# Kernel tuning notes

Measured on AMD Instinct MI355X. Metric: run time of the kernel, lower is better.

The kernel has to match this reference:

```python
import jax, jax.numpy as jnp
import numpy as np

C = 128; H = 56; W = 56; WS = 7; SS = 3; NH = 4; T = 8; B = 4
BT = B * T; L = H * W; N = WS * WS; HD = C // NH; SCALE = HD ** -0.5
NW = (H // WS) * (W // WS)

def _np_consts():
    # spatial relative position index (Swin)
    coords = np.stack(np.meshgrid(np.arange(WS), np.arange(WS), indexing='ij')).reshape(2, -1)
    rel = (coords[:, :, None] - coords[:, None, :]).transpose(1, 2, 0)
    rel[..., 0] += WS - 1; rel[..., 1] += WS - 1; rel[..., 0] *= 2 * WS - 1
    rpi = rel.sum(-1)  # (N, N) in [0, (2WS-1)^2)
    # temporal relative index
    tri = (np.arange(T)[:, None] - np.arange(T)[None, :]) + T - 1  # (T, T)
    # shifted-window attention mask
    img = np.zeros((1, H, W, 1), np.float32); cnt = 0
    sl = (slice(0, -WS), slice(-WS, -SS), slice(-SS, None))
    for hs in sl:
        for ws_ in sl:
            img[:, hs, ws_, :] = cnt; cnt += 1
    mw = img.reshape(1, H // WS, WS, W // WS, WS, 1).transpose(0, 1, 3, 2, 4, 5).reshape(-1, N)
    am = mw[:, None, :] - mw[:, :, None]
    attn_mask = np.where(am != 0, -100.0, 0.0).astype(np.float32)  # (NW, N, N)
    return rpi, tri, attn_mask

RPI, TRI, ATTN_MASK_NP = _np_consts()

def _ln(x, g, b, eps=1e-5):
    m = x.mean(-1, keepdims=True)
    v = ((x - m) ** 2).mean(-1, keepdims=True)
    return (x - m) * jax.lax.rsqrt(v + eps) * g + b

def _attn(x, bias, mask, qkv_w, qkv_b, proj_w, proj_b):
    # x: (Bn, n, C); bias: (NH, n, n); mask: (NW, n, n) or None
    Bn, n, _ = x.shape
    qkv = (x @ qkv_w + qkv_b).reshape(Bn, n, 3, NH, HD).transpose(2, 0, 3, 1, 4)
    q, k, v = qkv[0] * SCALE, qkv[1], qkv[2]  # (Bn, NH, n, HD)
    a = jnp.einsum('bhnd,bhmd->bhnm', q, k) + bias[None]
    if mask is not None:
        nW = mask.shape[0]
        a = (a.reshape(Bn // nW, nW, NH, n, n) + mask[None, :, None]).reshape(Bn, NH, n, n)
    a = jax.nn.softmax(a, axis=-1)
    o = jnp.einsum('bhnm,bhmd->bhnd', a, v).transpose(0, 2, 1, 3).reshape(Bn, n, C)
    return o @ proj_w + proj_b

def _fwd(x, qkv_w, qkv_b, proj_w, proj_b, rpb_table, tpb_table,
         norm1_g, norm1_b, norm2_g, norm2_b,
         mlp_w1, mlp_b1, mlp_w2, mlp_b2,
         s_w1, s_b1, s_w2, s_b2,
         t_w1, t_b1, t_w2, t_b2,
         a_w1, a_b1, a_w2, a_b2):
    gelu = lambda z: jax.nn.gelu(z, approximate=False)
    mask = jnp.asarray(ATTN_MASK_NP)
    sp_bias = rpb_table[RPI.reshape(-1)].reshape(N, N, NH).transpose(2, 0, 1)  # (NH,N,N)
    tp_bias = tpb_table[TRI.reshape(-1)].reshape(T, T, NH).transpose(2, 0, 1)  # (NH,T,T)

    # ---- temporal attention (t_attn=True, signal='video') ----
    shortcut = x
    xt = x.reshape(B, T, L, C).transpose(0, 2, 1, 3).reshape(B * L, T, C)
    xt = _ln(xt, norm1_g, norm1_b)
    xt = _attn(xt, tp_bias, None, qkv_w, qkv_b, proj_w, proj_b)
    # T_Adapter (non-residual)
    xt = gelu(xt @ t_w1 + t_b1) @ t_w2 + t_b2
    xt = xt.reshape(B, L, T, C).transpose(0, 2, 1, 3).reshape(BT, L, C)
    x = shortcut + xt

    # ---- shifted-window spatial attention ----
    shortcut = x
    xs = _ln(x, norm1_g, norm1_b).reshape(BT, H, W, C)
    xs = jnp.roll(xs, (-SS, -SS), axis=(1, 2))
    # window partition -> (BT*NW, N, C)
    xw = xs.reshape(BT, H // WS, WS, W // WS, WS, C).transpose(0, 1, 3, 2, 4, 5).reshape(-1, N, C)
    aw = _attn(xw, sp_bias, mask, qkv_w, qkv_b, proj_w, proj_b)
    # S_Adapter (SAdapter2, residual inside)
    aw = aw + (gelu(aw @ s_w1 + s_b1) @ s_w2 + s_b2)
    # window reverse
    xs = aw.reshape(BT, H // WS, W // WS, WS, WS, C).transpose(0, 1, 3, 2, 4, 5).reshape(BT, H, W, C)
    xs = jnp.roll(xs, (SS, SS), axis=(1, 2)).reshape(BT, L, C)
    x = shortcut + xs

    # ---- MLP + MLP_Adapter (AIM-style, scaled 0.5) ----
    xn = _ln(x, norm2_g, norm2_b)
    mlp = (gelu(xn @ mlp_w1 + mlp_b1)) @ mlp_w2 + mlp_b2
    ada = (gelu(xn @ a_w1 + a_b1)) @ a_w2 + a_b2
    return x + mlp + 0.5 * ada

def setup_inputs() -> dict:
    key = jax.random.key(0)
    ks = iter(jax.random.split(key, 16))
    p = lambda *s: jax.random.normal(next(ks), s, jnp.float32) * 0.02
    Ah = C // 4; M = 4 * C
    return {
        'x': jax.random.normal(next(ks), (BT, L, C), jnp.float32),
        'qkv_w': p(C, 3 * C), 'qkv_b': jnp.zeros((3 * C,), jnp.float32),
        'proj_w': p(C, C), 'proj_b': jnp.zeros((C,), jnp.float32),
        'rpb_table': p((2 * WS - 1) ** 2, NH), 'tpb_table': p(2 * T - 1, NH),
        'norm1_g': jnp.ones((C,), jnp.float32), 'norm1_b': jnp.zeros((C,), jnp.float32),
        'norm2_g': jnp.ones((C,), jnp.float32), 'norm2_b': jnp.zeros((C,), jnp.float32),
        'mlp_w1': p(C, M), 'mlp_b1': jnp.zeros((M,), jnp.float32),
        'mlp_w2': p(M, C), 'mlp_b2': jnp.zeros((C,), jnp.float32),
        's_w1': p(C, Ah), 's_b1': jnp.zeros((Ah,), jnp.float32),
        's_w2': p(Ah, C), 's_b2': jnp.zeros((C,), jnp.float32),
        't_w1': p(C, Ah), 't_b1': jnp.zeros((Ah,), jnp.float32),
        't_w2': p(Ah, C), 't_b2': jnp.zeros((C,), jnp.float32),
        'a_w1': p(C, Ah), 'a_b1': jnp.zeros((Ah,), jnp.float32),
        'a_w2': p(Ah, C), 'a_b2': jnp.zeros((C,), jnp.float32),
    }

def reference(x, qkv_w, qkv_b, proj_w, proj_b, rpb_table, tpb_table,
              norm1_g, norm1_b, norm2_g, norm2_b,
              mlp_w1, mlp_b1, mlp_w2, mlp_b2,
              s_w1, s_b1, s_w2, s_b2,
              t_w1, t_b1, t_w2, t_b2,
              a_w1, a_b1, a_w2, a_b2):
    return _fwd(x, qkv_w, qkv_b, proj_w, proj_b, rpb_table, tpb_table,
                norm1_g, norm1_b, norm2_g, norm2_b,
                mlp_w1, mlp_b1, mlp_w2, mlp_b2,
                s_w1, s_b1, s_w2, s_b2,
                t_w1, t_b1, t_w2, t_b2,
                a_w1, a_b1, a_w2, a_b2)
```

## Files before the change

### kernel.cpp

```cpp
#include <hip/hip_runtime.h>

#define TOKS 100352
#define LDIM 3136
#define SCALE_F 0.17677669529663687f

typedef unsigned short u16;
typedef u16   u16x8 __attribute__((ext_vector_type(8)));
typedef short s16x8 __attribute__((ext_vector_type(8)));
typedef float f32x8 __attribute__((ext_vector_type(8)));
typedef float f32x4 __attribute__((ext_vector_type(4)));

__device__ __forceinline__ float bf2f(u16 u){ return __uint_as_float(((unsigned)u)<<16); }
__device__ __forceinline__ u16 f2bf(float f){
  unsigned u = __float_as_uint(f);
  return (u16)((u + 0x7FFFu + ((u>>16)&1u)) >> 16);
}
__device__ __forceinline__ unsigned cvtpk(float a, float b){
  unsigned r;
  asm("v_cvt_pk_bf16_f32 %0, %1, %2" : "=v"(r) : "v"(a), "v"(b));
  return r;
}
__device__ __forceinline__ f32x8 ldbf8(const u16* p){
  u16x8 u = *(const u16x8*)p;
  f32x8 f;
  #pragma unroll
  for (int j=0;j<8;j++) f[j] = bf2f(u[j]);
  return f;
}
__device__ __forceinline__ u16x8 pack8(f32x8 v){
  u16x8 r;
  #pragma unroll
  for (int j=0;j<8;j++) r[j] = f2bf(v[j]);
  return r;
}
__device__ __forceinline__ float sum8(f32x8 a){
  return ((a[0]+a[1])+(a[2]+a[3]))+((a[4]+a[5])+(a[6]+a[7]));
}
__device__ __forceinline__ float gelu_f(float x){
  return x / (1.0f + __expf(-1.702f*x));
}

__device__ __forceinline__ void gl16(const u16* g, u16* l){
  __builtin_amdgcn_global_load_lds(
      (const __attribute__((address_space(1))) unsigned*)(const void*)g,
      (__attribute__((address_space(3))) unsigned*)(void*)l, 16, 0, 0);
}
__device__ __forceinline__ void stage_tile(const u16* __restrict__ src, size_t rowstart,
    int KTOT, int koff, u16* lds, int wv, int lane){
  const int rr = wv*4 + (lane>>4);
  const int sl = lane&15;
  const int kb = sl ^ (rr&7);
  const u16* g0 = src + (rowstart + rr)*(size_t)KTOT + koff + kb*8;
  u16* l0 = lds + wv*4*128;
  #pragma unroll
  for (int it=0; it<8; it++)
    gl16(g0 + (size_t)it*16*KTOT, l0 + it*16*128);
}

struct WSrc { const float* p[10]; };
__global__ __launch_bounds__(256) void prep_w(WSrc s, u16* __restrict__ dst){
  const int Ks[10]={128,128,128,512,128,32,128,32,128,32};
  const int Ns[10]={384,128,512,128,32,128,32,128,32,128};
  const int off[11]={0,49152,65536,131072,196608,200704,204800,208896,212992,217088,221184};
  int idx = blockIdx.x*256+threadIdx.x;
  int m=0;
  #pragma unroll
  for (int i=0;i<10;i++) if (idx>=off[i+1]) m=i+1;
  int e = idx-off[m];
  int K=Ks[m], Nn=Ns[m];
  int n=e/K, k=e-n*K;
  dst[idx] = f2bf(s.p[m][k*Nn+n]);
}

__global__ __launch_bounds__(256) void ln_kernel(const float* __restrict__ x,
    const float* __restrict__ g, const float* __restrict__ bta, u16* __restrict__ out)
{
  int tok  = (int)((blockIdx.x*256u + threadIdx.x) >> 6);
  int lane = threadIdx.x & 63;
  const float* xr = x + (size_t)tok*128;
  float v0 = xr[lane], v1 = xr[lane+64];
  float s = v0+v1;
  #pragma unroll
  for (int o=32;o;o>>=1) s += __shfl_xor(s,o);
  float m = s*(1.0f/128.0f);
  float d0=v0-m, d1=v1-m;
  float q = d0*d0+d1*d1;
  #pragma unroll
  for (int o=32;o;o>>=1) q += __shfl_xor(q,o);
  float rs = rsqrtf(q*(1.0f/128.0f)+1e-5f);
  u16* orow = out + (size_t)tok*128;
  orow[lane]    = f2bf(d0*rs*g[lane]   + bta[lane]);
  orow[lane+64] = f2bf(d1*rs*g[lane+64]+ bta[lane+64]);
}

template<int KCH, int NTC, int EPI>
__global__ __launch_bounds__(256,2) void gemm_tile(
    const u16* __restrict__ X, const u16* __restrict__ WT,
    const float* __restrict__ bias, void* outp, int N,
    const float* res1, const u16* __restrict__ adab)
{
  constexpr int KTOT = KCH*128;
  __shared__ u16 As[128*128];
  __shared__ u16 Bs[128*128];
  const int tid = threadIdx.x;
  const int wv = tid>>6, lane = tid&63, lr = lane>>4, lc = lane&15;
  const int wr = wv>>1, wc = wv&1;
  const size_t row0 = (size_t)blockIdx.x*128;

  f32x4 acc[4][4];
  #pragma unroll
  for (int mi=0;mi<4;mi++)
    #pragma unroll
    for (int nj=0;nj<4;nj++) acc[mi][nj] = (f32x4){0.f,0.f,0.f,0.f};

  for (int kc=0; kc<KCH; kc++){
    for (int nt=0; nt<NTC; nt++){
      if (kc+nt > 0) __syncthreads();
      if (nt == 0) stage_tile(X, row0, KTOT, kc*128, As, wv, lane);
      stage_tile(WT, (size_t)nt*128, KTOT, kc*128, Bs, wv, lane);
      __syncthreads();
      #pragma unroll
      for (int kt=0; kt<4; kt++){
        s16x8 af[4], bfr[4];
        #pragma unroll
        for (int mi=0;mi<4;mi++){
          int row = wr*64 + mi*16 + lc;
          af[mi] = *(const s16x8*)&As[row*128 + (((kt*4+lr) ^ (lc&7))*8)];
        }
        #pragma unroll
        for (int nj=0;nj<4;nj++){
          int col = wc*64 + nj*16 + lc;
          bfr[nj] = *(const s16x8*)&Bs[col*128 + (((kt*4+lr) ^ (lc&7))*8)];
        }
        #pragma unroll
        for (int mi=0;mi<4;mi++)
          #pragma unroll
          for (int nj=0;nj<4;nj++)
            acc[mi][nj] = __builtin_amdgcn_mfma_f32_16x16x32_bf16(bfr[nj], af[mi], acc[mi][nj], 0,0,0);
      }
      {
        #pragma unroll
        for (int nj=0;nj<4;nj++){
          const int colb = nt*128 + wc*64 + nj*16 + lr*4;
          float4 b4 = *(const float4*)&bias[colb];
          #pragma unroll
          for (int mi=0;mi<4;mi++){
            const size_t row = row0 + wr*64 + mi*16 + lc;
            float v0=acc[mi][nj][0]+b4.x, v1=acc[mi][nj][1]+b4.y,
                  v2=acc[mi][nj][2]+b4.z, v3=acc[mi][nj][3]+b4.w;
            if constexpr (EPI==1){ v0=gelu_f(v0); v1=gelu_f(v1); v2=gelu_f(v2); v3=gelu_f(v3); }
            uint2 pk; pk.x = cvtpk(v0,v1); pk.y = cvtpk(v2,v3);
            *(uint2*)&((u16*)outp)[row*(size_t)N + colb] = pk;
            acc[mi][nj] = (f32x4){0.f,0.f,0.f,0.f};
          }
        }
      }
    }
  }
  (void)res1; (void)adab;
}

template<int SMODE>
__global__ __launch_bounds__(256,2) void proj_ada_tile(
    const u16* __restrict__ O, const u16* __restrict__ PW, const float* __restrict__ pb,
    const u16* __restrict__ W1T, const float* __restrict__ b1,
    const u16* __restrict__ W2T, const float* __restrict__ b2,
    const float* __restrict__ res1, float* __restrict__ outp,
    const float* __restrict__ gn, const float* __restrict__ gb, u16* __restrict__ xnout)
{
  __shared__ u16 As[128*128];
  __shared__ u16 Bs[128*128];
  __shared__ u16 Hs[4][32][40];
  const int tid = threadIdx.x;
  const int wv = tid>>6, lane = tid&63, lr = lane>>4, lc = lane&15;
  const int wr = wv>>1, wc = wv&1;
  const size_t row0 = (size_t)blockIdx.x*128;
  stage_tile(O, row0, 128, 0, As, wv, lane);
  stage_tile(PW, 0, 128, 0, Bs, wv, lane);
  __syncthreads();
  f32x4 acc[4][4];
  #pragma unroll
  for (int mi=0;mi<4;mi++)
    #pragma unroll
    for (int nj=0;nj<4;nj++) acc[mi][nj] = (f32x4){0.f,0.f,0.f,0.f};
  #pragma unroll
  for (int kt=0; kt<4; kt++){
    s16x8 af[4], bfr[4];
    #pragma unroll
    for (int mi=0;mi<4;mi++)
      af[mi] = *(const s16x8*)&As[(wr*64+mi*16+lc)*128 + (((kt*4+lr) ^ (lc&7))*8)];
    #pragma unroll
    for (int nj=0;nj<4;nj++)
      bfr[nj] = *(const s16x8*)&Bs[(wc*64+nj*16+lc)*128 + (((kt*4+lr) ^ (lc&7))*8)];
    #pragma unroll
    for (int mi=0;mi<4;mi++)
      #pragma unroll
      for (int nj=0;nj<4;nj++)
        acc[mi][nj] = __builtin_amdgcn_mfma_f32_16x16x32_bf16(bfr[nj], af[mi], acc[mi][nj], 0,0,0);
  }
  __syncthreads();
  #pragma unroll
  for (int nj=0;nj<4;nj++){
    const int colb = wc*64 + nj*16 + lr*4;
    float4 b4 = *(const float4*)&pb[colb];
    #pragma unroll
    for (int mi=0;mi<4;mi++){
      const int row = wr*64 + mi*16 + lc;
      uint2 pk;
      pk.x = cvtpk(acc[mi][nj][0]+b4.x, acc[mi][nj][1]+b4.y);
      pk.y = cvtpk(acc[mi][nj][2]+b4.z, acc[mi][nj][3]+b4.w);
      *(uint2*)&As[row*128 + (((colb>>3) ^ (row&7))*8) + (colb&7)] = pk;
    }
  }
  __syncthreads();
  const int rbase = wv*32;
  f32x4 a2[2][2];
  #pragma unroll
  for (int mi=0;mi<2;mi++){ a2[mi][0]=(f32x4){0.f,0.f,0.f,0.f}; a2[mi][1]=(f32x4){0.f,0.f,0.f,0.f}; }
  #pragma unroll
  for (int kt=0; kt<4; kt++){
    s16x8 af0 = *(const s16x8*)&As[(rbase+lc)*128 + (((kt*4+lr) ^ (lc&7))*8)];
    s16x8 af1 = *(const s16x8*)&As[(rbase+16+lc)*128 + (((kt*4+lr) ^ (lc&7))*8)];
    #pragma unroll
    for (int nj=0; nj<2; nj++){
      s16x8 b = *(const s16x8*)&W1T[(size_t)(nj*16+lc)*128 + kt*32 + lr*8];
      a2[0][nj] = __builtin_amdgcn_mfma_f32_16x16x32_bf16(b, af0, a2[0][nj], 0,0,0);
      a2[1][nj] = __builtin_amdgcn_mfma_f32_16x16x32_bf16(b, af1, a2[1][nj], 0,0,0);
    }
  }
  #pragma unroll
  for (int nj=0;nj<2;nj++){
    const int hb = nj*16 + lr*4;
    float4 b4 = *(const float4*)&b1[hb];
    #pragma unroll
    for (int mi=0;mi<2;mi++){
      const int tok = mi*16 + lc;
      uint2 pk;
      pk.x = cvtpk(gelu_f(a2[mi][nj][0]+b4.x), gelu_f(a2[mi][nj][1]+b4.y));
      pk.y = cvtpk(gelu_f(a2[mi][nj][2]+b4.z), gelu_f(a2[mi][nj][3]+b4.w));
      *(uint2*)&Hs[wv][tok][hb] = pk;
    }
  }
  f32x4 a3[2][8];
  #pragma unroll
  for (int mi=0;mi<2;mi++){
    s16x8 af = *(const s16x8*)&Hs[wv][mi*16+lc][lr*8];
    #pragma unroll
    for (int nj=0;nj<8;nj++){
      s16x8 b = *(const s16x8*)&W2T[(size_t)(nj*16+lc)*32 + lr*8];
      a3[mi][nj] = __builtin_amdgcn_mfma_f32_16x16x32_bf16(b, af, (f32x4){0.f,0.f,0.f,0.f}, 0,0,0);
    }
  }
  float sum[2]={0.f,0.f}, sq[2]={0.f,0.f};
  #pragma unroll
  for (int mi=0;mi<2;mi++){
    const int rl = rbase + mi*16 + lc;
    const size_t row = row0 + rl;
    #pragma unroll
    for (int nj=0;nj<8;nj++){
      const int colb = nj*16 + lr*4;
      float4 b4 = *(const float4*)&b2[colb];
      float4 r4 = *(const float4*)&res1[row*128 + colb];
      f32x4 v;
      v[0]=a3[mi][nj][0]+b4.x+r4.x; v[1]=a3[mi][nj][1]+b4.y+r4.y;
      v[2]=a3[mi][nj][2]+b4.z+r4.z; v[3]=a3[mi][nj][3]+b4.w+r4.w;
      if constexpr (SMODE==1){
        uint2 pu = *(const uint2*)&As[rl*128 + (((colb>>3) ^ (rl&7))*8) + (colb&7)];
        v[0] += bf2f((u16)(pu.x&0xffff)); v[1] += bf2f((u16)(pu.x>>16));
        v[2] += bf2f((u16)(pu.y&0xffff)); v[3] += bf2f((u16)(pu.y>>16));
      }
      float4 st; st.x=v[0]; st.y=v[1]; st.z=v[2]; st.w=v[3];
      *(float4*)&outp[row*128 + colb] = st;
      a3[mi][nj] = v;
      sum[mi] += (v[0]+v[1])+(v[2]+v[3]);
      sq[mi]  += (v[0]*v[0]+v[1]*v[1])+(v[2]*v[2]+v[3]*v[3]);
    }
  }
  #pragma unroll
  for (int mi=0;mi<2;mi++){
    float s2 = sum[mi], q2 = sq[mi];
    s2 += __shfl_xor(s2,16); s2 += __shfl_xor(s2,32);
    q2 += __shfl_xor(q2,16); q2 += __shfl_xor(q2,32);
    float mean = s2*(1.0f/128.0f);
    float var  = q2*(1.0f/128.0f) - mean*mean;
    float rs   = rsqrtf(var + 1e-5f);
    const size_t row = row0 + rbase + mi*16 + lc;
    #pragma unroll
    for (int nj=0;nj<8;nj++){
      const int colb = nj*16 + lr*4;
      float4 g4 = *(const float4*)&gn[colb];
      float4 h4 = *(const float4*)&gb[colb];
      uint2 pk;
      pk.x = cvtpk((a3[mi][nj][0]-mean)*rs*g4.x + h4.x,
                   (a3[mi][nj][1]-mean)*rs*g4.y + h4.y);
      pk.y = cvtpk((a3[mi][nj][2]-mean)*rs*g4.z + h4.z,
                   (a3[mi][nj][3]-mean)*rs*g4.w + h4.w);
      *(uint2*)&xnout[row*128 + colb] = pk;
    }
  }
}

__global__ __launch_bounds__(256,2) void mlp_fused(
    const u16* __restrict__ X, const u16* __restrict__ W1T, const float* __restrict__ b1,
    const u16* __restrict__ W2T, const float* __restrict__ b2,
    const u16* __restrict__ A1T, const float* __restrict__ ab1,
    const u16* __restrict__ A2T, const float* __restrict__ ab2,
    float* __restrict__ outp)
{
  __shared__ u16 As[128*128];
  __shared__ u16 Bs[128*128];
  const int tid = threadIdx.x;
  const int wv = tid>>6, lane = tid&63, lr = lane>>4, lc = lane&15;
  const int wr = wv>>1, wc = wv&1;
  const size_t row0 = (size_t)blockIdx.x*128;

  stage_tile(X, row0, 128, 0, As, wv, lane);
  stage_tile(W1T, 0, 128, 0, Bs, wv, lane);
  __syncthreads();

  f32x4 oacc[4][4];
  #pragma unroll
  for (int mi=0;mi<4;mi++)
    #pragma unroll
    for (int nj=0;nj<4;nj++) oacc[mi][nj] = (f32x4){0.f,0.f,0.f,0.f};

  for (int ck=0; ck<4; ck++){
    f32x4 acc[4][4];
    #pragma unroll
    for (int mi=0;mi<4;mi++)
      #pragma unroll
      for (int nj=0;nj<4;nj++) acc[mi][nj] = (f32x4){0.f,0.f,0.f,0.f};
    #pragma unroll
    for (int kt=0; kt<4; kt++){
      s16x8 af[4], bfr[4];
      #pragma unroll
      for (int mi=0;mi<4;mi++)
        af[mi] = *(const s16x8*)&As[(wr*64+mi*16+lc)*128 + (((kt*4+lr) ^ (lc&7))*8)];
      #pragma unroll
      for (int nj=0;nj<4;nj++)
        bfr[nj] = *(const s16x8*)&Bs[(wc*64+nj*16+lc)*128 + (((kt*4+lr) ^ (lc&7))*8)];
      #pragma unroll
      for (int mi=0;mi<4;mi++)
        #pragma unroll
        for (int nj=0;nj<4;nj++)
          acc[mi][nj] = __builtin_amdgcn_mfma_f32_16x16x32_bf16(bfr[nj], af[mi], acc[mi][nj], 0,0,0);
    }
    __syncthreads();
    #pragma unroll
    for (int nj=0;nj<4;nj++){
      const int hidb = wc*64 + nj*16 + lr*4;
      float4 b4 = *(const float4*)&b1[ck*128 + hidb];
      #pragma unroll
      for (int mi=0;mi<4;mi++){
        const int tok = wr*64 + mi*16 + lc;
        uint2 pk;
        pk.x = cvtpk(gelu_f(acc[mi][nj][0]+b4.x), gelu_f(acc[mi][nj][1]+b4.y));
        pk.y = cvtpk(gelu_f(acc[mi][nj][2]+b4.z), gelu_f(acc[mi][nj][3]+b4.w));
        *(uint2*)&Bs[tok*128 + (((hidb>>3) ^ (tok&7))*8) + (hidb&7)] = pk;
      }
    }
    __syncthreads();
    #pragma unroll
    for (int kt=0; kt<4; kt++){
      s16x8 hf[4], wf[4];
      #pragma unroll
      for (int mi=0;mi<4;mi++)
        hf[mi] = *(const s16x8*)&Bs[(wr*64+mi*16+lc)*128 + (((kt*4+lr) ^ (lc&7))*8)];
      #pragma unroll
      for (int nj=0;nj<4;nj++)
        wf[nj] = *(const s16x8*)&W2T[(size_t)(wc*64+nj*16+lc)*512 + ck*128 + kt*32 + lr*8];
      #pragma unroll
      for (int mi=0;mi<4;mi++)
        #pragma unroll
        for (int nj=0;nj<4;nj++)
          oacc[mi][nj] = __builtin_amdgcn_mfma_f32_16x16x32_bf16(hf[mi], wf[nj], oacc[mi][nj], 0,0,0);
    }
    if (ck<3){
      __syncthreads();
      stage_tile(W1T, (size_t)(ck+1)*128, 128, 0, Bs, wv, lane);
      __syncthreads();
    }
  }

  f32x4 a2[4][2];
  #pragma unroll
  for (int mi=0;mi<4;mi++){ a2[mi][0]=(f32x4){0.f,0.f,0.f,0.f}; a2[mi][1]=(f32x4){0.f,0.f,0.f,0.f}; }
  #pragma unroll
  for (int kt=0; kt<4; kt++){
    s16x8 af[4];
    #pragma unroll
    for (int mi=0;mi<4;mi++)
      af[mi] = *(const s16x8*)&As[(wr*64+mi*16+lc)*128 + (((kt*4+lr) ^ (lc&7))*8)];
    s16x8 bA = *(const s16x8*)&A1T[(size_t)lc*128 + kt*32 + lr*8];
    s16x8 bB = *(const s16x8*)&A1T[(size_t)(16+lc)*128 + kt*32 + lr*8];
    #pragma unroll
    for (int mi=0;mi<4;mi++){
      a2[mi][0] = __builtin_amdgcn_mfma_f32_16x16x32_bf16(bA, af[mi], a2[mi][0], 0,0,0);
      a2[mi][1] = __builtin_amdgcn_mfma_f32_16x16x32_bf16(bB, af[mi], a2[mi][1], 0,0,0);
    }
  }
  __syncthreads();
  if (wc==0){
    #pragma unroll
    for (int nj=0;nj<2;nj++){
      const int hb = nj*16 + lr*4;
      float4 b4 = *(const float4*)&ab1[hb];
      #pragma unroll
      for (int mi=0;mi<4;mi++){
        const int tok = wr*64 + mi*16 + lc;
        uint2 pk;
        pk.x = cvtpk(0.5f*gelu_f(a2[mi][nj][0]+b4.x), 0.5f*gelu_f(a2[mi][nj][1]+b4.y));
        pk.y = cvtpk(0.5f*gelu_f(a2[mi][nj][2]+b4.z), 0.5f*gelu_f(a2[mi][nj][3]+b4.w));
        *(uint2*)&As[tok*64 + (((hb>>3) ^ (tok&7))*8) + (hb&7)] = pk;
      }
    }
  }
  __syncthreads();
  {
    s16x8 hqf[4];
    #pragma unroll
    for (int mi=0;mi<4;mi++){
      const int tok = wr*64 + mi*16 + lc;
      hqf[mi] = *(const s16x8*)&As[tok*64 + ((lr ^ (tok&7))*8)];
    }
    #pragma unroll
    for (int nj=0;nj<4;nj++){
      s16x8 a2f = *(const s16x8*)&A2T[(size_t)(wc*64+nj*16+lc)*32 + lr*8];
      #pragma unroll
      for (int mi=0;mi<4;mi++)
        oacc[mi][nj] = __builtin_amdgcn_mfma_f32_16x16x32_bf16(hqf[mi], a2f, oacc[mi][nj], 0,0,0);
    }
  }
  #pragma unroll
  for (int nj=0;nj<4;nj++){
    const int col = wc*64 + nj*16 + lc;
    const float badd = b2[col] + 0.5f*ab2[col];
    #pragma unroll
    for (int mi=0;mi<4;mi++){
      #pragma unroll
      for (int r=0;r<4;r++){
        const size_t row = row0 + wr*64 + mi*16 + lr*4 + r;
        outp[row*128 + col] += oacc[mi][nj][r] + badd;
      }
    }
  }
}

__global__ __launch_bounds__(256) void t_attn_kernel(const u16* __restrict__ qkv,
    const float* __restrict__ tpb, u16* __restrict__ o)
{
  const int tid = threadIdx.x;
  const int li = tid>>5, h = (tid>>3)&3, t = tid&7;
  const int b = blockIdx.x/392, lt = blockIdx.x%392;
  const int l = lt*8+li;
  const size_t rowt = (size_t)(b*8+t)*LDIM + l;
  const u16* qp = qkv + rowt*384 + h*32;
  f32x8 q0 = ldbf8(qp)   *SCALE_F, q1 = ldbf8(qp+8) *SCALE_F,
        q2 = ldbf8(qp+16)*SCALE_F, q3 = ldbf8(qp+24)*SCALE_F;
  float s[8];
  #pragma unroll
  for (int t2=0;t2<8;t2++){
    const u16* kp = qkv + ((size_t)(b*8+t2)*LDIM + l)*384 + 128 + h*32;
    f32x8 d = q0*ldbf8(kp) + q1*ldbf8(kp+8) + q2*ldbf8(kp+16) + q3*ldbf8(kp+24);
    s[t2] = sum8(d) + tpb[(t-t2+7)*4 + h];
  }
  float m = s[0];
  #pragma unroll
  for (int t2=1;t2<8;t2++) m = fmaxf(m, s[t2]);
  float ssum = 0.f;
  #pragma unroll
  for (int t2=0;t2<8;t2++){ s[t2] = __expf(s[t2]-m); ssum += s[t2]; }
  const float inv = 1.0f/ssum;
  f32x8 o0={0,0,0,0,0,0,0,0}, o1={0,0,0,0,0,0,0,0},
        o2={0,0,0,0,0,0,0,0}, o3={0,0,0,0,0,0,0,0};
  #pragma unroll
  for (int t2=0;t2<8;t2++){
    const u16* vp = qkv + ((size_t)(b*8+t2)*LDIM + l)*384 + 256 + h*32;
    float aw = s[t2]*inv;
    o0 += aw*ldbf8(vp); o1 += aw*ldbf8(vp+8); o2 += aw*ldbf8(vp+16); o3 += aw*ldbf8(vp+24);
  }
  u16* op = o + rowt*128 + h*32;
  *(u16x8*)op      = pack8(o0); *(u16x8*)(op+8)  = pack8(o1);
  *(u16x8*)(op+16) = pack8(o2); *(u16x8*)(op+24) = pack8(o3);
}

__global__ __launch_bounds__(256,2) void s_attn_mfma(const u16* __restrict__ qkv,
    const float* __restrict__ rpb, u16* __restrict__ o)
{
  __shared__ u16 Qs[64][136];
  __shared__ u16 Ks[64][136];
  __shared__ u16 Vt[128][72];
  __shared__ float rpbL[676];
  __shared__ int rowL[49];
  __shared__ int codeL[49];
  const int tid = threadIdx.x;
  const int bidx = blockIdx.x;
  const int bt = bidx>>6, wh = (bidx>>3)&7, ww = bidx&7;
  if (tid < 49){
    int ph = tid/7, pwv = tid%7;
    int rh = wh*7+ph, rw = ww*7+pwv;
    int oh = rh+3; if (oh>=56) oh-=56;
    int ow = rw+3; if (ow>=56) ow-=56;
    rowL[tid] = bt*LDIM + oh*56 + ow;
    codeL[tid] = ((rh<49)?0:((rh<53)?1:2))*3 + ((rw<49)?0:((rw<53)?1:2));
  }
  for (int i2 = tid; i2 < 676; i2 += 256) rpbL[i2] = rpb[i2];
  for (int idx = tid; idx < 128*15; idx += 256){
    int d = idx/15, jj = 49 + (idx - d*15);
    Vt[d][jj] = 0;
  }
  __syncthreads();
  #pragma unroll
  for (int it = 0; it < 10; it++){
    int idx = it*256 + tid;
    if (idx < 2352){
      int j = idx/48, s = idx - j*48;
      const u16* src = qkv + (size_t)rowL[j]*384 + s*8;
      u16x8 v = *(const u16x8*)src;
      if (s < 16)      *(u16x8*)&Qs[j][s*8] = v;
      else if (s < 32) *(u16x8*)&Ks[j][(s-16)*8] = v;
      else { int c0 = (s-32)*8;
        #pragma unroll
        for (int e=0;e<8;e++) Vt[c0+e][j] = v[e];
      }
    }
  }
  __syncthreads();

  const int h = tid>>6, lane = tid&63, lr = lane>>4, lc = lane&15;
  s16x8 qf[4], kf[4];
  #pragma unroll
  for (int t=0;t<4;t++){
    qf[t] = *(const s16x8*)&Qs[t*16+lc][h*32+lr*8];
    kf[t] = *(const s16x8*)&Ks[t*16+lc][h*32+lr*8];
  }
  f32x4 sa[4][4];
  #pragma unroll
  for (int tj=0;tj<4;tj++){
    #pragma unroll
    for (int ti=0;ti<4;ti++)
      sa[tj][ti] = __builtin_amdgcn_mfma_f32_16x16x32_bf16(kf[tj], qf[ti], (f32x4){0.f,0.f,0.f,0.f}, 0,0,0);
  }
  int ihv[4], iwv[4], civ[4];
  #pragma unroll
  for (int ti=0;ti<4;ti++){
    int i = ti*16+lc; int im = (i<49)? i:48;
    int ih2 = (im*147)>>10; ihv[ti]=ih2; iwv[ti]=im-ih2*7; civ[ti]=codeL[im];
  }
  float rs[4] = {0.f,0.f,0.f,0.f};
  #pragma unroll
  for (int tj=0;tj<4;tj++){
    #pragma unroll
    for (int r=0;r<4;r++){
      int j = tj*16 + lr*4 + r;
      bool jv = (j<49);
      int jm = jv? j:48;
      int jh2 = (jm*147)>>10; int jw2 = jm - jh2*7; int cj = codeL[jm];
      #pragma unroll
      for (int ti=0;ti<4;ti++){
        float sv = sa[tj][ti][r]*SCALE_F
                 + rpbL[((ihv[ti]-jh2+6)*13 + (iwv[ti]-jw2+6))*4 + h];
        if (civ[ti] != cj) sv -= 100.f;
        float pv = jv ? __expf(sv) : 0.f;
        sa[tj][ti][r] = pv;
        rs[ti] += pv;
      }
    }
  }
  #pragma unroll
  for (int ti=0;ti<4;ti++){
    float t2 = rs[ti];
    t2 += __shfl_xor(t2, 16);
    t2 += __shfl_xor(t2, 32);
    rs[ti] = 1.0f/t2;
  }
  unsigned lo[4][4], hi[4][4];
  #pragma unroll
  for (int tj=0;tj<4;tj++){
    #pragma unroll
    for (int ti=0;ti<4;ti++){
      float inv = rs[ti];
      lo[tj][ti] = cvtpk(sa[tj][ti][0]*inv, sa[tj][ti][1]*inv);
      hi[tj][ti] = cvtpk(sa[tj][ti][2]*inv, sa[tj][ti][3]*inv);
    }
  }
  f32x4 oa[4][2];
  #pragma unroll
  for (int mi=0;mi<4;mi++){ oa[mi][0]=(f32x4){0.f,0.f,0.f,0.f}; oa[mi][1]=(f32x4){0.f,0.f,0.f,0.f}; }
  const int srcA = lc + ((lane>>4)&1)*32;
  const int srcB = srcA + 16;
  const bool hiHalf = (lr>=2);
  #pragma unroll
  for (int kt=0;kt<2;kt++){
    s16x8 vf[2];
    #pragma unroll
    for (int nd=0;nd<2;nd++)
      vf[nd] = *(const s16x8*)&Vt[h*32 + nd*16 + lc][kt*32 + lr*8];
    #pragma unroll
    for (int mi=0;mi<4;mi++){
      unsigned wA0 = __shfl(lo[2*kt][mi],   srcA), wB0 = __shfl(lo[2*kt+1][mi], srcA);
      unsigned wA1 = __shfl(hi[2*kt][mi],   srcA), wB1 = __shfl(hi[2*kt+1][mi], srcA);
      unsigned wA2 = __shfl(lo[2*kt][mi],   srcB), wB2 = __shfl(lo[2*kt+1][mi], srcB);
      unsigned wA3 = __shfl(hi[2*kt][mi],   srcB), wB3 = __shfl(hi[2*kt+1][mi], srcB);
      union { unsigned u[4]; s16x8 v8; } cv;
      cv.u[0] = hiHalf? wB0 : wA0;
      cv.u[1] = hiHalf? wB1 : wA1;
      cv.u[2] = hiHalf? wB2 : wA2;
      cv.u[3] = hiHalf? wB3 : wA3;
      #pragma unroll
      for (int nd=0;nd<2;nd++)
        oa[mi][nd] = __builtin_amdgcn_mfma_f32_16x16x32_bf16(cv.v8, vf[nd], oa[mi][nd], 0,0,0);
    }
  }
  #pragma unroll
  for (int mi=0;mi<4;mi++){
    #pragma unroll
    for (int r=0;r<4;r++){
      int i = mi*16 + lr*4 + r;
      if (i < 49){
        size_t orow = (size_t)rowL[i]*128 + h*32;
        o[orow + lc]      = f2bf(oa[mi][0][r]);
        o[orow + 16 + lc] = f2bf(oa[mi][1][r]);
      }
    }
  }
}

extern "C" void kernel_launch(void* const* d_in, const int* in_sizes, int n_in,
                              void* d_out, int out_size, void* d_ws, size_t ws_size,
                              hipStream_t stream)
{
  (void)in_sizes; (void)n_in; (void)out_size; (void)ws_size;
  const float* x      = (const float*)d_in[0];
  const float* qkv_w  = (const float*)d_in[1];
  const float* qkv_b  = (const float*)d_in[2];
  const float* proj_w = (const float*)d_in[3];
  const float* proj_b = (const float*)d_in[4];
  const float* rpb    = (const float*)d_in[5];
  const float* tpb    = (const float*)d_in[6];
  const float* n1g    = (const float*)d_in[7];
  const float* n1b    = (const float*)d_in[8];
  const float* n2g    = (const float*)d_in[9];
  const float* n2b    = (const float*)d_in[10];
  const float* mw1    = (const float*)d_in[11];
  const float* mb1    = (const float*)d_in[12];
  const float* mw2    = (const float*)d_in[13];
  const float* mb2    = (const float*)d_in[14];
  const float* sw1    = (const float*)d_in[15];
  const float* sb1    = (const float*)d_in[16];
  const float* sw2    = (const float*)d_in[17];
  const float* sb2    = (const float*)d_in[18];
  const float* tw1    = (const float*)d_in[19];
  const float* tb1    = (const float*)d_in[20];
  const float* tw2    = (const float*)d_in[21];
  const float* tb2    = (const float*)d_in[22];
  const float* aw1    = (const float*)d_in[23];
  const float* ab1    = (const float*)d_in[24];
  const float* aw2    = (const float*)d_in[25];
  const float* ab2    = (const float*)d_in[26];

  char* ws = (char*)d_ws;
  u16*   Xn  = (u16*)(ws);
  u16*   QKV = (u16*)(ws + 25690112ULL);
  u16*   O   = (u16*)(ws + 102760448ULL);
  float* Cb  = (float*)(ws + 134873088ULL);
  u16*   WT  = (u16*)(ws + 186253312ULL);
  float* out = (float*)d_out;

  const u16 *WTqkv=WT, *WTproj=WT+49152, *WTm1=WT+65536, *WTm2=WT+131072,
            *WTt1=WT+196608, *WTt2=WT+200704, *WTs1=WT+204800, *WTs2=WT+208896,
            *WTa1=WT+212992, *WTa2=WT+217088;

  WSrc srcs; srcs.p[0]=qkv_w; srcs.p[1]=proj_w; srcs.p[2]=mw1; srcs.p[3]=mw2;
  srcs.p[4]=tw1; srcs.p[5]=tw2; srcs.p[6]=sw1; srcs.p[7]=sw2; srcs.p[8]=aw1; srcs.p[9]=aw2;
  prep_w<<<864,256,0,stream>>>(srcs, WT);

  ln_kernel<<<25088,256,0,stream>>>(x, n1g, n1b, Xn);
  gemm_tile<1,3,0><<<784,256,0,stream>>>(Xn, WTqkv, qkv_b, QKV, 384, nullptr,nullptr);
  t_attn_kernel<<<1568,256,0,stream>>>(QKV, tpb, O);
  proj_ada_tile<0><<<784,256,0,stream>>>(O, WTproj, proj_b, WTt1, tb1, WTt2, tb2,
                                          x, Cb, n1g, n1b, Xn);
  gemm_tile<1,3,0><<<784,256,0,stream>>>(Xn, WTqkv, qkv_b, QKV, 384, nullptr,nullptr);
  s_attn_mfma<<<2048,256,0,stream>>>(QKV, rpb, O);
  proj_ada_tile<1><<<784,256,0,stream>>>(O, WTproj, proj_b, WTs1, sb1, WTs2, sb2,
                                          Cb, out, n2g, n2b, Xn);
  mlp_fused<<<784,256,0,stream>>>(Xn, WTm1, mb1, WTm2, mb2, WTa1, ab1, WTa2, ab2, out);
}
```

Measured before the change: 378.6 us.

## Read GEMM weight fragments directly from global memory instead of staging in LDS

The QKV GEMM and the MLP first-layer GEMM now load weight fragments straight from global memory (L2-resident) instead of staging each weight tile into shared memory. This removes a 32KB LDS buffer and several barriers, so the QKV kernel's launch bound rises to 3 blocks per SM. The MLP kernel also gets a separate small buffer for the adapter hidden activations, and its final residual accumulation swaps MFMA operand order so output can be written as vectorized float4 read-modify-writes rather than scalar strided updates. In exchange, weight reads lose LDS reuse across waves and depend on cache hit rates.

Result: slower. 467.7 us (+23.5%).

```diff
diff --git a/kernel.cpp b/kernel.cpp
--- a/kernel.cpp
+++ b/kernel.cpp
@@ -93,71 +93,54 @@
   orow[lane+64] = f2bf(d1*rs*g[lane+64]+ bta[lane+64]);
 }
 
-template<int KCH, int NTC, int EPI>
-__global__ __launch_bounds__(256,2) void gemm_tile(
+template<int NTC>
+__global__ __launch_bounds__(256,3) void gemm_qkv(
     const u16* __restrict__ X, const u16* __restrict__ WT,
-    const float* __restrict__ bias, void* outp, int N,
-    const float* res1, const u16* __restrict__ adab)
+    const float* __restrict__ bias, u16* __restrict__ outp, int N)
 {
-  constexpr int KTOT = KCH*128;
   __shared__ u16 As[128*128];
-  __shared__ u16 Bs[128*128];
   const int tid = threadIdx.x;
   const int wv = tid>>6, lane = tid&63, lr = lane>>4, lc = lane&15;
   const int wr = wv>>1, wc = wv&1;
   const size_t row0 = (size_t)blockIdx.x*128;
-
-  f32x4 acc[4][4];
-  #pragma unroll
-  for (int mi=0;mi<4;mi++)
-    #pragma unroll
-    for (int nj=0;nj<4;nj++) acc[mi][nj] = (f32x4){0.f,0.f,0.f,0.f};
-
-  for (int kc=0; kc<KCH; kc++){
-    for (int nt=0; nt<NTC; nt++){
-      if (kc+nt > 0) __syncthreads();
-      if (nt == 0) stage_tile(X, row0, KTOT, kc*128, As, wv, lane);
-      stage_tile(WT, (size_t)nt*128, KTOT, kc*128, Bs, wv, lane);
-      __syncthreads();
-      #pragma unroll
-      for (int kt=0; kt<4; kt++){
-        s16x8 af[4], bfr[4];
+  stage_tile(X, row0, 128, 0, As, wv, lane);
+  __syncthreads();
+
+  for (int nt=0; nt<NTC; nt++){
+    f32x4 acc[4][4];
+    #pragma unroll
+    for (int mi=0;mi<4;mi++)
+      #pragma unroll
+      for (int nj=0;nj<4;nj++) acc[mi][nj] = (f32x4){0.f,0.f,0.f,0.f};
+    #pragma unroll
+    for (int kt=0; kt<4; kt++){
+      s16x8 af[4], wf[4];
+      #pragma unroll
+      for (int mi=0;mi<4;mi++)
+        af[mi] = *(const s16x8*)&As[(wr*64+mi*16+lc)*128 + (((kt*4+lr) ^ (lc&7))*8)];
+      #pragma unroll
+      for (int nj=0;nj<4;nj++)
+        wf[nj] = *(const s16x8*)&WT[(size_t)(nt*128 + wc*64+nj*16+lc)*128 + kt*32 + lr*8];
+      #pragma unroll
+      for (int mi=0;mi<4;mi++)
         #pragma unroll
-        for (int mi=0;mi<4;mi++){
-          int row = wr*64 + mi*16 + lc;
-          af[mi] = *(const s16x8*)&As[row*128 + (((kt*4+lr) ^ (lc&7))*8)];
-        }
-        #pragma unroll
-        for (int nj=0;nj<4;nj++){
-          int col = wc*64 + nj*16 + lc;
-          bfr[nj] = *(const s16x8*)&Bs[col*128 + (((kt*4+lr) ^ (lc&7))*8)];
-        }
-        #pragma unroll
-        for (int mi=0;mi<4;mi++)
-          #pragma unroll
-          for (int nj=0;nj<4;nj++)
-            acc[mi][nj] = __builtin_amdgcn_mfma_f32_16x16x32_bf16(bfr[nj], af[mi], acc[mi][nj], 0,0,0);
+        for (int nj=0;nj<4;nj++)
+          acc[mi][nj] = __builtin_amdgcn_mfma_f32_16x16x32_bf16(wf[nj], af[mi], acc[mi][nj], 0,0,0);
+    }
+    #pragma unroll
+    for (int nj=0;nj<4;nj++){
+      const int colb = nt*128 + wc*64 + nj*16 + lr*4;
+      float4 b4 = *(const float4*)&bias[colb];
+      #pragma unroll
+      for (int mi=0;mi<4;mi++){
+        const size_t row = row0 + wr*64 + mi*16 + lc;
+        uint2 pk;
+        pk.x = cvtpk(acc[mi][nj][0]+b4.x, acc[mi][nj][1]+b4.y);
+        pk.y = cvtpk(acc[mi][nj][2]+b4.z, acc[mi][nj][3]+b4.w);
+        *(uint2*)&outp[row*(size_t)N + colb] = pk;
       }
-      {
-        #pragma unroll
-        for (int nj=0;nj<4;nj++){
-          const int colb = nt*128 + wc*64 + nj*16 + lr*4;
-          float4 b4 = *(const float4*)&bias[colb];
-          #pragma unroll
-          for (int mi=0;mi<4;mi++){
-            const size_t row = row0 + wr*64 + mi*16 + lc;
-            float v0=acc[mi][nj][0]+b4.x, v1=acc[mi][nj][1]+b4.y,
-                  v2=acc[mi][nj][2]+b4.z, v3=acc[mi][nj][3]+b4.w;
-            if constexpr (EPI==1){ v0=gelu_f(v0); v1=gelu_f(v1); v2=gelu_f(v2); v3=gelu_f(v3); }
-            uint2 pk; pk.x = cvtpk(v0,v1); pk.y = cvtpk(v2,v3);
-            *(uint2*)&((u16*)outp)[row*(size_t)N + colb] = pk;
-            acc[mi][nj] = (f32x4){0.f,0.f,0.f,0.f};
-          }
-        }
-      }
-    }
-  }
-  (void)res1; (void)adab;
+    }
+  }
 }
 
 template<int SMODE>
@@ -308,14 +291,14 @@
     float* __restrict__ outp)
 {
   __shared__ u16 As[128*128];
-  __shared__ u16 Bs[128*128];
+  __shared__ u16 Hb[128*128];
+  __shared__ u16 Hq[128*40];
   const int tid = threadIdx.x;
   const int wv = tid>>6, lane = tid&63, lr = lane>>4, lc = lane&15;
   const int wr = wv>>1, wc = wv&1;
   const size_t row0 = (size_t)blockIdx.x*128;
 
   stage_tile(X, row0, 128, 0, As, wv, lane);
-  stage_tile(W1T, 0, 128, 0, Bs, wv, lane);
   __syncthreads();
 
   f32x4 oacc[4][4];
@@ -332,18 +315,18 @@
       for (int nj=0;nj<4;nj++) acc[mi][nj] = (f32x4){0.f,0.f,0.f,0.f};
     #pragma unroll
     for (int kt=0; kt<4; kt++){
-      s16x8 af[4], bfr[4];
+      s16x8 af[4], wf[4];
       #pragma unroll
       for (int mi=0;mi<4;mi++)
         af[mi] = *(const s16x8*)&As[(wr*64+mi*16+lc)*128 + (((kt*4+lr) ^ (lc&7))*8)];
       #pragma unroll
       for (int nj=0;nj<4;nj++)
-        bfr[nj] = *(const s16x8*)&Bs[(wc*64+nj*16+lc)*128 + (((kt*4+lr) ^ (lc&7))*8)];
+        wf[nj] = *(const s16x8*)&W1T[(size_t)(ck*128 + wc*64+nj*16+lc)*128 + kt*32 + lr*8];
       #pragma unroll
       for (int mi=0;mi<4;mi++)
         #pragma unroll
         for (int nj=0;nj<4;nj++)
-          acc[mi][nj] = __builtin_amdgcn_mfma_f32_16x16x32_bf16(bfr[nj], af[mi], acc[mi][nj], 0,0,0);
+          acc[mi][nj] = __builtin_amdgcn_mfma_f32_16x16x32_bf16(wf[nj], af[mi], acc[mi][nj], 0,0,0);
     }
     __syncthreads();
     #pragma unroll
@@ -356,7 +339,7 @@
         uint2 pk;
         pk.x = cvtpk(gelu_f(acc[mi][nj][0]+b4.x), gelu_f(acc[mi][nj][1]+b4.y));
         pk.y = cvtpk(gelu_f(acc[mi][nj][2]+b4.z), gelu_f(acc[mi][nj][3]+b4.w));
-        *(uint2*)&Bs[tok*128 + (((hidb>>3) ^ (tok&7))*8) + (hidb&7)] = pk;
+        *(uint2*)&Hb[tok*128 + (((hidb>>3) ^ (tok&7))*8) + (hidb&7)] = pk;
       }
     }
     __syncthreads();
@@ -365,7 +348,7 @@
       s16x8 hf[4], wf[4];
       #pragma unroll
       for (int mi=0;mi<4;mi++)
-        hf[mi] = *(const s16x8*)&Bs[(wr*64+mi*16+lc)*128 + (((kt*4+lr) ^ (lc&7))*8)];
+        hf[mi] = *(const s16x8*)&Hb[(wr*64+mi*16+lc)*128 + (((kt*4+lr) ^ (lc&7))*8)];
       #pragma unroll
       for (int nj=0;nj<4;nj++)
         wf[nj] = *(const s16x8*)&W2T[(size_t)(wc*64+nj*16+lc)*512 + ck*128 + kt*32 + lr*8];
@@ -373,12 +356,7 @@
       for (int mi=0;mi<4;mi++)
         #pragma unroll
         for (int nj=0;nj<4;nj++)
-          oacc[mi][nj] = __builtin_amdgcn_mfma_f32_16x16x32_bf16(hf[mi], wf[nj], oacc[mi][nj], 0,0,0);
-    }
-    if (ck<3){
-      __syncthreads();
-      stage_tile(W1T, (size_t)(ck+1)*128, 128, 0, Bs, wv, lane);
-      __syncthreads();
+          oacc[mi][nj] = __builtin_amdgcn_mfma_f32_16x16x32_bf16(wf[nj], hf[mi], oacc[mi][nj], 0,0,0);
     }
   }
 
@@ -399,7 +377,6 @@
       a2[mi][1] = __builtin_amdgcn_mfma_f32_16x16x32_bf16(bB, af[mi], a2[mi][1], 0,0,0);
     }
   }
-  __syncthreads();
   if (wc==0){
     #pragma unroll
     for (int nj=0;nj<2;nj++){
@@ -411,7 +388,7 @@
         uint2 pk;
         pk.x = cvtpk(0.5f*gelu_f(a2[mi][nj][0]+b4.x), 0.5f*gelu_f(a2[mi][nj][1]+b4.y));
         pk.y = cvtpk(0.5f*gelu_f(a2[mi][nj][2]+b4.z), 0.5f*gelu_f(a2[mi][nj][3]+b4.w));
-        *(uint2*)&As[tok*64 + (((hb>>3) ^ (tok&7))*8) + (hb&7)] = pk;
+        *(uint2*)&Hq[tok*40 + hb] = pk;
       }
     }
   }
@@ -419,29 +396,31 @@
   {
     s16x8 hqf[4];
     #pragma unroll
-    for (int mi=0;mi<4;mi++){
-      const int tok = wr*64 + mi*16 + lc;
-      hqf[mi] = *(const s16x8*)&As[tok*64 + ((lr ^ (tok&7))*8)];
-    }
+    for (int mi=0;mi<4;mi++)
+      hqf[mi] = *(const s16x8*)&Hq[(wr*64+mi*16+lc)*40 + lr*8];
     #pragma unroll
     for (int nj=0;nj<4;nj++){
       s16x8 a2f = *(const s16x8*)&A2T[(size_t)(wc*64+nj*16+lc)*32 + lr*8];
       #pragma unroll
       for (int mi=0;mi<4;mi++)
-        oacc[mi][nj] = __builtin_amdgcn_mfma_f32_16x16x32_bf16(hqf[mi], a2f, oacc[mi][nj], 0,0,0);
+        oacc[mi][nj] = __builtin_amdgcn_mfma_f32_16x16x32_bf16(a2f, hqf[mi], oacc[mi][nj], 0,0,0);
     }
   }
   #pragma unroll
   for (int nj=0;nj<4;nj++){
-    const int col = wc*64 + nj*16 + lc;
-    const float badd = b2[col] + 0.5f*ab2[col];
+    const int colb = wc*64 + nj*16 + lr*4;
+    float4 b4 = *(const float4*)&b2[colb];
+    float4 a4 = *(const float4*)&ab2[colb];
     #pragma unroll
     for (int mi=0;mi<4;mi++){
-      #pragma unroll
-      for (int r=0;r<4;r++){
-        const size_t row = row0 + wr*64 + mi*16 + lr*4 + r;
-        outp[row*128 + col] += oacc[mi][nj][r] + badd;
-      }
+      const size_t row = row0 + wr*64 + mi*16 + lc;
+      float4 o4 = *(const float4*)&outp[row*128 + colb];
+      float4 v;
+      v.x = o4.x + oacc[mi][nj][0] + b4.x + 0.5f*a4.x;
+      v.y = o4.y + oacc[mi][nj][1] + b4.y + 0.5f*a4.y;
+      v.z = o4.z + oacc[mi][nj][2] + b4.z + 0.5f*a4.z;
+      v.w = o4.w + oacc[mi][nj][3] + b4.w + 0.5f*a4.w;
+      *(float4*)&outp[row*128 + colb] = v;
     }
   }
 }
@@ -676,11 +655,11 @@
   prep_w<<<864,256,0,stream>>>(srcs, WT);
 
   ln_kernel<<<25088,256,0,stream>>>(x, n1g, n1b, Xn);
-  gemm_tile<1,3,0><<<784,256,0,stream>>>(Xn, WTqkv, qkv_b, QKV, 384, nullptr,nullptr);
+  gemm_qkv<3><<<784,256,0,stream>>>(Xn, WTqkv, qkv_b, QKV, 384);
   t_attn_kernel<<<1568,256,0,stream>>>(QKV, tpb, O);
   proj_ada_tile<0><<<784,256,0,stream>>>(O, WTproj, proj_b, WTt1, tb1, WTt2, tb2,
                                           x, Cb, n1g, n1b, Xn);
-  gemm_tile<1,3,0><<<784,256,0,stream>>>(Xn, WTqkv, qkv_b, QKV, 384, nullptr,nullptr);
+  gemm_qkv<3><<<784,256,0,stream>>>(Xn, WTqkv, qkv_b, QKV, 384);
   s_attn_mfma<<<2048,256,0,stream>>>(QKV, rpb, O);
   proj_ada_tile<1><<<784,256,0,stream>>>(O, WTproj, proj_b, WTs1, sb1, WTs2, sb2,
                                           Cb, out, n2g, n2b, Xn);
```

## Restructure fused MLP so each wave owns 32 tokens with register-held inputs

Applied to the files above, without the earlier changes.

The fused MLP kernel now assigns each wave a private 32-token slice. Each wave keeps its X fragments in registers instead of staging them in shared memory, and writes its GELU hidden activations to a per-wave padded LDS buffer. This removes the X shared tile and several block-wide barriers, and lets the next W1 chunk be staged while the GELU epilogue and second GEMM run. The output accumulation switches to transposed MFMA operands so the residual add uses float4 read-modify-write. In exchange, each wave must read all of W1 and W2 for its tokens, so W2 global reads per block grow, and register pressure rises with the 8x2 accumulators.

Result: slower. 400.8 us (+5.9%).

```diff
diff --git a/kernel.cpp b/kernel.cpp
--- a/kernel.cpp
+++ b/kernel.cpp
@@ -307,141 +307,133 @@
     const u16* __restrict__ A2T, const float* __restrict__ ab2,
     float* __restrict__ outp)
 {
-  __shared__ u16 As[128*128];
   __shared__ u16 Bs[128*128];
+  __shared__ u16 Hw[4][32][136];
   const int tid = threadIdx.x;
   const int wv = tid>>6, lane = tid&63, lr = lane>>4, lc = lane&15;
-  const int wr = wv>>1, wc = wv&1;
   const size_t row0 = (size_t)blockIdx.x*128;
-
-  stage_tile(X, row0, 128, 0, As, wv, lane);
+  const int tokb = wv*32;
+
+  s16x8 xf[4][2];
+  #pragma unroll
+  for (int kt=0; kt<4; kt++)
+    #pragma unroll
+    for (int mi=0; mi<2; mi++)
+      xf[kt][mi] = *(const s16x8*)&X[(row0 + tokb + mi*16 + lc)*128 + kt*32 + lr*8];
+
   stage_tile(W1T, 0, 128, 0, Bs, wv, lane);
-  __syncthreads();
-
-  f32x4 oacc[4][4];
-  #pragma unroll
-  for (int mi=0;mi<4;mi++)
-    #pragma unroll
-    for (int nj=0;nj<4;nj++) oacc[mi][nj] = (f32x4){0.f,0.f,0.f,0.f};
+
+  f32x4 oacc[8][2];
+  #pragma unroll
+  for (int cj=0;cj<8;cj++)
+    #pragma unroll
+    for (int ti=0;ti<2;ti++) oacc[cj][ti] = (f32x4){0.f,0.f,0.f,0.f};
 
   for (int ck=0; ck<4; ck++){
-    f32x4 acc[4][4];
-    #pragma unroll
-    for (int mi=0;mi<4;mi++)
-      #pragma unroll
-      for (int nj=0;nj<4;nj++) acc[mi][nj] = (f32x4){0.f,0.f,0.f,0.f};
+    __syncthreads();
+    f32x4 acc[2][8];
+    #pragma unroll
+    for (int mi=0;mi<2;mi++)
+      #pragma unroll
+      for (int nj=0;nj<8;nj++) acc[mi][nj] = (f32x4){0.f,0.f,0.f,0.f};
     #pragma unroll
     for (int kt=0; kt<4; kt++){
-      s16x8 af[4], bfr[4];
-      #pragma unroll
-      for (int mi=0;mi<4;mi++)
-        af[mi] = *(const s16x8*)&As[(wr*64+mi*16+lc)*128 + (((kt*4+lr) ^ (lc&7))*8)];
-      #pragma unroll
-      for (int nj=0;nj<4;nj++)
-        bfr[nj] = *(const s16x8*)&Bs[(wc*64+nj*16+lc)*128 + (((kt*4+lr) ^ (lc&7))*8)];
-      #pragma unroll
-      for (int mi=0;mi<4;mi++)
+      s16x8 wf[8];
+      #pragma unroll
+      for (int nj=0;nj<8;nj++)
+        wf[nj] = *(const s16x8*)&Bs[(nj*16+lc)*128 + (((kt*4+lr) ^ (lc&7))*8)];
+      #pragma unroll
+      for (int mi=0;mi<2;mi++)
         #pragma unroll
-        for (int nj=0;nj<4;nj++)
-          acc[mi][nj] = __builtin_amdgcn_mfma_f32_16x16x32_bf16(bfr[nj], af[mi], acc[mi][nj], 0,0,0);
+        for (int nj=0;nj<8;nj++)
+          acc[mi][nj] = __builtin_amdgcn_mfma_f32_16x16x32_bf16(wf[nj], xf[kt][mi], acc[mi][nj], 0,0,0);
     }
     __syncthreads();
-    #pragma unroll
-    for (int nj=0;nj<4;nj++){
-      const int hidb = wc*64 + nj*16 + lr*4;
-      float4 b4 = *(const float4*)&b1[ck*128 + hidb];
-      #pragma unroll
-      for (int mi=0;mi<4;mi++){
-        const int tok = wr*64 + mi*16 + lc;
+    if (ck < 3) stage_tile(W1T, (size_t)(ck+1)*128, 128, 0, Bs, wv, lane);
+    #pragma unroll
+    for (int nj=0;nj<8;nj++){
+      const int hb = nj*16 + lr*4;
+      float4 b4 = *(const float4*)&b1[ck*128 + hb];
+      #pragma unroll
+      for (int mi=0;mi<2;mi++){
+        const int tok = mi*16 + lc;
         uint2 pk;
         pk.x = cvtpk(gelu_f(acc[mi][nj][0]+b4.x), gelu_f(acc[mi][nj][1]+b4.y));
         pk.y = cvtpk(gelu_f(acc[mi][nj][2]+b4.z), gelu_f(acc[mi][nj][3]+b4.w));
-        *(uint2*)&Bs[tok*128 + (((hidb>>3) ^ (tok&7))*8) + (hidb&7)] = pk;
+        *(uint2*)&Hw[wv][tok][hb] = pk;
       }
     }
-    __syncthreads();
     #pragma unroll
     for (int kt=0; kt<4; kt++){
-      s16x8 hf[4], wf[4];
-      #pragma unroll
-      for (int mi=0;mi<4;mi++)
-        hf[mi] = *(const s16x8*)&Bs[(wr*64+mi*16+lc)*128 + (((kt*4+lr) ^ (lc&7))*8)];
-      #pragma unroll
-      for (int nj=0;nj<4;nj++)
-        wf[nj] = *(const s16x8*)&W2T[(size_t)(wc*64+nj*16+lc)*512 + ck*128 + kt*32 + lr*8];
-      #pragma unroll
-      for (int mi=0;mi<4;mi++)
+      s16x8 hf[2], wf2[8];
+      #pragma unroll
+      for (int ti=0;ti<2;ti++)
+        hf[ti] = *(const s16x8*)&Hw[wv][ti*16+lc][kt*32 + lr*8];
+      #pragma unroll
+      for (int cj=0;cj<8;cj++)
+        wf2[cj] = *(const s16x8*)&W2T[(size_t)(cj*16+lc)*512 + ck*128 + kt*32 + lr*8];
+      #pragma unroll
+      for (int cj=0;cj<8;cj++)
         #pragma unroll
-        for (int nj=0;nj<4;nj++)
-          oacc[mi][nj] = __builtin_amdgcn_mfma_f32_16x16x32_bf16(hf[mi], wf[nj], oacc[mi][nj], 0,0,0);
-    }
-    if (ck<3){
-      __syncthreads();
-      stage_tile(W1T, (size_t)(ck+1)*128, 128, 0, Bs, wv, lane);
-      __syncthreads();
-    }
-  }
-
-  f32x4 a2[4][2];
-  #pragma unroll
-  for (int mi=0;mi<4;mi++){ a2[mi][0]=(f32x4){0.f,0.f,0.f,0.f}; a2[mi][1]=(f32x4){0.f,0.f,0.f,0.f}; }
+        for (int ti=0;ti<2;ti++)
+          oacc[cj][ti] = __builtin_amdgcn_mfma_f32_16x16x32_bf16(wf2[cj], hf[ti], oacc[cj][ti], 0,0,0);
+    }
+  }
+
+  f32x4 a2[2][2];
+  #pragma unroll
+  for (int mi=0;mi<2;mi++){ a2[mi][0]=(f32x4){0.f,0.f,0.f,0.f}; a2[mi][1]=(f32x4){0.f,0.f,0.f,0.f}; }
   #pragma unroll
   for (int kt=0; kt<4; kt++){
-    s16x8 af[4];
-    #pragma unroll
-    for (int mi=0;mi<4;mi++)
-      af[mi] = *(const s16x8*)&As[(wr*64+mi*16+lc)*128 + (((kt*4+lr) ^ (lc&7))*8)];
     s16x8 bA = *(const s16x8*)&A1T[(size_t)lc*128 + kt*32 + lr*8];
     s16x8 bB = *(const s16x8*)&A1T[(size_t)(16+lc)*128 + kt*32 + lr*8];
     #pragma unroll
-    for (int mi=0;mi<4;mi++){
-      a2[mi][0] = __builtin_amdgcn_mfma_f32_16x16x32_bf16(bA, af[mi], a2[mi][0], 0,0,0);
-      a2[mi][1] = __builtin_amdgcn_mfma_f32_16x16x32_bf16(bB, af[mi], a2[mi][1], 0,0,0);
-    }
-  }
-  __syncthreads();
-  if (wc==0){
-    #pragma unroll
-    for (int nj=0;nj<2;nj++){
-      const int hb = nj*16 + lr*4;
-      float4 b4 = *(const float4*)&ab1[hb];
-      #pragma unroll
-      for (int mi=0;mi<4;mi++){
-        const int tok = wr*64 + mi*16 + lc;
-        uint2 pk;
-        pk.x = cvtpk(0.5f*gelu_f(a2[mi][nj][0]+b4.x), 0.5f*gelu_f(a2[mi][nj][1]+b4.y));
-        pk.y = cvtpk(0.5f*gelu_f(a2[mi][nj][2]+b4.z), 0.5f*gelu_f(a2[mi][nj][3]+b4.w));
-        *(uint2*)&As[tok*64 + (((hb>>3) ^ (tok&7))*8) + (hb&7)] = pk;
-      }
-    }
-  }
-  __syncthreads();
+    for (int mi=0;mi<2;mi++){
+      a2[mi][0] = __builtin_amdgcn_mfma_f32_16x16x32_bf16(bA, xf[kt][mi], a2[mi][0], 0,0,0);
+      a2[mi][1] = __builtin_amdgcn_mfma_f32_16x16x32_bf16(bB, xf[kt][mi], a2[mi][1], 0,0,0);
+    }
+  }
+  #pragma unroll
+  for (int nj=0;nj<2;nj++){
+    const int hb = nj*16 + lr*4;
+    float4 b4 = *(const float4*)&ab1[hb];
+    #pragma unroll
+    for (int mi=0;mi<2;mi++){
+      const int tok = mi*16 + lc;
+      uint2 pk;
+      pk.x = cvtpk(0.5f*gelu_f(a2[mi][nj][0]+b4.x), 0.5f*gelu_f(a2[mi][nj][1]+b4.y));
+      pk.y = cvtpk(0.5f*gelu_f(a2[mi][nj][2]+b4.z), 0.5f*gelu_f(a2[mi][nj][3]+b4.w));
+      *(uint2*)&Hw[wv][tok][hb] = pk;
+    }
+  }
   {
-    s16x8 hqf[4];
-    #pragma unroll
-    for (int mi=0;mi<4;mi++){
-      const int tok = wr*64 + mi*16 + lc;
-      hqf[mi] = *(const s16x8*)&As[tok*64 + ((lr ^ (tok&7))*8)];
-    }
-    #pragma unroll
-    for (int nj=0;nj<4;nj++){
-      s16x8 a2f = *(const s16x8*)&A2T[(size_t)(wc*64+nj*16+lc)*32 + lr*8];
-      #pragma unroll
-      for (int mi=0;mi<4;mi++)
-        oacc[mi][nj] = __builtin_amdgcn_mfma_f32_16x16x32_bf16(hqf[mi], a2f, oacc[mi][nj], 0,0,0);
-    }
-  }
-  #pragma unroll
-  for (int nj=0;nj<4;nj++){
-    const int col = wc*64 + nj*16 + lc;
-    const float badd = b2[col] + 0.5f*ab2[col];
-    #pragma unroll
-    for (int mi=0;mi<4;mi++){
-      #pragma unroll
-      for (int r=0;r<4;r++){
-        const size_t row = row0 + wr*64 + mi*16 + lr*4 + r;
-        outp[row*128 + col] += oacc[mi][nj][r] + badd;
-      }
+    s16x8 hqf[2];
+    #pragma unroll
+    for (int ti=0;ti<2;ti++)
+      hqf[ti] = *(const s16x8*)&Hw[wv][ti*16+lc][lr*8];
+    #pragma unroll
+    for (int cj=0;cj<8;cj++){
+      s16x8 a2f = *(const s16x8*)&A2T[(size_t)(cj*16+lc)*32 + lr*8];
+      #pragma unroll
+      for (int ti=0;ti<2;ti++)
+        oacc[cj][ti] = __builtin_amdgcn_mfma_f32_16x16x32_bf16(a2f, hqf[ti], oacc[cj][ti], 0,0,0);
+    }
+  }
+  #pragma unroll
+  for (int cj=0;cj<8;cj++){
+    const int colb = cj*16 + lr*4;
+    float4 b4 = *(const float4*)&b2[colb];
+    float4 a4 = *(const float4*)&ab2[colb];
+    #pragma unroll
+    for (int ti=0;ti<2;ti++){
+      const size_t row = row0 + tokb + ti*16 + lc;
+      float4 o4 = *(const float4*)&outp[row*128 + colb];
+      float4 v;
+      v.x = o4.x + oacc[cj][ti][0] + b4.x + 0.5f*a4.x;
+      v.y = o4.y + oacc[cj][ti][1] + b4.y + 0.5f*a4.y;
+      v.z = o4.z + oacc[cj][ti][2] + b4.z + 0.5f*a4.z;
+      v.w = o4.w + oacc[cj][ti][3] + b4.w + 0.5f*a4.w;
+      *(float4*)&outp[row*128 + colb] = v;
     }
   }
 }
```
